# Kernel tuning notes

Hardware: AMD Instinct MI355X
Metric: run time of the kernel (lower is better)

The kernel has to match this reference:

```python
import jax, jax.numpy as jnp
import numpy as np
from jax import ops as jops

N = 20000          # nodes
E = 320000         # edges
IN_DIM = 16        # input_dim_features_extractor
HID = 64           # hidden_dim_features_extractor
HEADS = 4          # n_attention_heads
LAYERS = 2         # n_layers_features_extractor
NEG_SLOPE = 0.2    # DGL EGATConv leaky_relu slope


def setup_inputs() -> dict:
    key = jax.random.key(0)
    ks = jax.random.split(key, 16)
    s = lambda *sh: 1.0 / np.sqrt(sh[-2] if len(sh) >= 2 else sh[-1])
    inp = {
        "node_feat": jax.random.normal(ks[0], (N, IN_DIM), jnp.float32),
        "edge_feat": jax.random.normal(ks[1], (E, HID), jnp.float32),
        "src": jax.random.randint(ks[2], (E,), 0, N, jnp.int32),
        "dst": jax.random.randint(ks[3], (E,), 0, N, jnp.int32),
        # features_embedder (MLP n_layers=1 -> single Linear IN_DIM->HID)
        "W_embed": jax.random.normal(ks[4], (IN_DIM, HID), jnp.float32) * s(IN_DIM, HID),
        "b_embed": jnp.zeros((HID,), jnp.float32),
        # per-layer EGATConv params (stacked over layer dim)
        "W_ni": jax.random.normal(ks[5], (LAYERS, HID, HEADS * HID), jnp.float32) * s(HID, 1),
        "W_nj": jax.random.normal(ks[6], (LAYERS, HID, HEADS * HID), jnp.float32) * s(HID, 1),
        "W_fij": jax.random.normal(ks[7], (LAYERS, HID, HEADS * HID), jnp.float32) * s(HID, 1),
        "b_att": jnp.zeros((LAYERS, HEADS * HID), jnp.float32),
        "attn": jax.random.normal(ks[8], (LAYERS, HEADS, HID), jnp.float32) * s(HID),
        "W_node": jax.random.normal(ks[9], (LAYERS, HID, HEADS * HID), jnp.float32) * s(HID, 1),
        # per-layer MLP (n_layers=1 -> Linear HEADS*HID -> HID)
        "W_mlp": jax.random.normal(ks[10], (LAYERS, HEADS * HID, HID), jnp.float32) * s(HEADS * HID, 1),
        "b_mlp": jnp.zeros((LAYERS, HID), jnp.float32),
    }
    return inp


def _egat(h, f, src, dst, W_ni, W_nj, W_fij, b, attn, W_node):
    """DGL EGATConv: edge-feature attention + softmax-weighted aggregation."""
    # per-edge attention features: u_add_v + edge proj + bias
    f_ni = h @ W_ni                         # (N, H*D)
    f_nj = h @ W_nj                         # (N, H*D)
    f_fij = f @ W_fij                       # (E, H*D)
    f_out = f_ni[src] + f_nj[dst] + f_fij + b
    f_out = jax.nn.leaky_relu(f_out, NEG_SLOPE).reshape(E, HEADS, HID)
    e = jnp.einsum("ehd,hd->eh", f_out, attn)            # (E, H) logits
    # edge softmax over incoming edges of each dst node (numerically stable)
    m = jops.segment_max(e, dst, num_segments=N)          # (N, H)
    a = jnp.exp(e - m[dst])
    z = jops.segment_sum(a, dst, num_segments=N)          # (N, H)
    a = a / z[dst]
    # weighted message aggregation
    hn = (h @ W_node).reshape(N, HEADS, HID)
    msg = hn[src] * a[:, :, None]                         # (E, H, D)
    out = jops.segment_sum(msg, dst, num_segments=N)      # (N, H, D)
    return out


def reference(node_feat, edge_feat, src, dst, W_embed, b_embed,
              W_ni, W_nj, W_fij, b_att, attn, W_node, W_mlp, b_mlp):
    features_list = [node_feat]                 # layer_pooling='all'
    features = node_feat @ W_embed + b_embed    # features_embedder
    features_list.append(features)
    for L in range(LAYERS):
        h = _egat(features, edge_feat, src, dst,
                  W_ni[L], W_nj[L], W_fij[L], b_att[L], attn[L], W_node[L])
        new = h.reshape(N, HEADS * HID) @ W_mlp[L] + b_mlp[L]
        features = new + features               # residual
        features_list.append(features)
    return jnp.concatenate(features_list, axis=-1)   # (N, 16 + 3*64)
```

## Files before the change

kernel.cpp:

```cpp
#include <hip/hip_runtime.h>
#include <math.h>

#define NN 20000
#define NE 320000
#define IN_DIM 16
#define HID 64
#define HEADS 4
#define HD 256
#define OUTW 208
#define NEG 0.2f

typedef unsigned short u16;
typedef unsigned int u32;
typedef __attribute__((ext_vector_type(8))) short bf16x8;
typedef __attribute__((ext_vector_type(4))) float f32x4;

__device__ __forceinline__ float b2f(u16 u) {
  union { u32 i; float f; } c; c.i = ((u32)u) << 16; return c.f;
}
__device__ __forceinline__ u16 f2b(float f) {
  union { float f; u32 i; } c; c.f = f;
  u32 r = (c.i + 0x7FFFu + ((c.i >> 16) & 1u)) >> 16;
  return (u16)r;
}

__global__ void k_embed(const float* __restrict__ nf, const float* __restrict__ We,
                        const float* __restrict__ be, float* __restrict__ feat,
                        float* __restrict__ out) {
  int tid = blockIdx.x * blockDim.x + threadIdx.x;
  int n = tid >> 6, c = tid & 63;
  if (n >= NN) return;
  float acc = be[c];
#pragma unroll
  for (int k = 0; k < IN_DIM; ++k)
    acc += nf[n * IN_DIM + k] * We[k * HID + c];
  feat[n * HID + c] = acc;
  out[n * OUTW + 16 + c] = acc;
  if (c < IN_DIM) out[n * OUTW + c] = nf[n * IN_DIM + c];
}

__global__ void k_count(const int* __restrict__ dst, int* __restrict__ counts) {
  int e = blockIdx.x * blockDim.x + threadIdx.x;
  if (e < NE) atomicAdd(&counts[dst[e]], 1);
}

__global__ void k_scan(const int* __restrict__ counts, int* __restrict__ rowptr) {
  __shared__ int wsum[16];
  __shared__ int tot;
  int lane = threadIdx.x & 63, wid = threadIdx.x >> 6;
  int running = 0;
  if (threadIdx.x == 0) rowptr[0] = 0;
  for (int base = 0; base < NN; base += 1024) {
    int i = base + threadIdx.x;
    int x = (i < NN) ? counts[i] : 0;
#pragma unroll
    for (int d = 1; d < 64; d <<= 1) {
      int t = __shfl_up(x, d);
      if (lane >= d) x += t;
    }
    if (lane == 63) wsum[wid] = x;
    __syncthreads();
    if (wid == 0) {
      int wv = (lane < 16) ? wsum[lane] : 0;
#pragma unroll
      for (int d = 1; d < 16; d <<= 1) {
        int t = __shfl_up(wv, d);
        if (lane >= d) wv += t;
      }
      if (lane < 16) wsum[lane] = wv;
      if (lane == 15) tot = wv;
    }
    __syncthreads();
    int wpre = (wid == 0) ? 0 : wsum[wid - 1];
    if (i < NN) rowptr[i + 1] = running + wpre + x;
    running += tot;
    __syncthreads();
  }
}

__global__ void k_scatter(const int* __restrict__ dst, const int* __restrict__ src,
                          const int* __restrict__ rowptr, int* __restrict__ cursor,
                          int* __restrict__ eidx, int* __restrict__ srcp,
                          int* __restrict__ dstp) {
  int e = blockIdx.x * blockDim.x + threadIdx.x;
  if (e >= NE) return;
  int d = dst[e];
  int pos = rowptr[d] + atomicAdd(&cursor[d], 1);
  eidx[pos] = e;
  srcp[pos] = src[e];
  dstp[pos] = d;
}

__global__ void k_permute(const float* __restrict__ ef, const int* __restrict__ eidx,
                          u16* __restrict__ efbp) {
  int t = blockIdx.x * blockDim.x + threadIdx.x;
  int slot = t >> 4, c = (t & 15) * 4;
  int e = eidx[slot];
  float4 v = *reinterpret_cast<const float4*>(&ef[(size_t)e * HID + c]);
  ushort4 o;
  o.x = f2b(v.x); o.y = f2b(v.y); o.z = f2b(v.z); o.w = f2b(v.w);
  *reinterpret_cast<ushort4*>(&efbp[(size_t)slot * HID + c]) = o;
}

__global__ void k_prepw(const float* __restrict__ Wf, u16* __restrict__ Wt) {
  int tid = blockIdx.x * blockDim.x + threadIdx.x;
  int n = tid >> 6, k = tid & 63;
  if (n >= HD) return;
  Wt[n * HID + k] = f2b(Wf[k * HD + n]);
}

__global__ __launch_bounds__(256) void k_nodeproj(
    const float* __restrict__ feat, const float* __restrict__ Wni,
    const float* __restrict__ Wnj, const float* __restrict__ Wnd,
    const float* __restrict__ batt, u16* __restrict__ fni,
    u16* __restrict__ fnj, u16* __restrict__ hn) {
  __shared__ float hs[8 * HID];
  int n0 = blockIdx.x * 8;
  int c = threadIdx.x;
  for (int i = threadIdx.x; i < 8 * HID; i += 256)
    hs[i] = feat[(size_t)(n0 + (i >> 6)) * HID + (i & 63)];
  __syncthreads();
  float aI[8] = {0}, aJ[8] = {0}, aN[8] = {0};
  for (int k = 0; k < HID; ++k) {
    float wi = Wni[k * HD + c], wj = Wnj[k * HD + c], wn = Wnd[k * HD + c];
#pragma unroll
    for (int t = 0; t < 8; ++t) {
      float x = hs[t * HID + k];
      aI[t] += x * wi; aJ[t] += x * wj; aN[t] += x * wn;
    }
  }
  float b = batt[c];
#pragma unroll
  for (int t = 0; t < 8; ++t) {
    int n = n0 + t;
    fni[(size_t)n * HD + c] = f2b(aI[t] + b);
    fnj[(size_t)n * HD + c] = f2b(aJ[t]);
    hn[(size_t)n * HD + c]  = f2b(aN[t]);
  }
}

__global__ __launch_bounds__(256) void k_edgelogits(
    const u16* __restrict__ efbp, const int* __restrict__ srcp,
    const int* __restrict__ dstp, const u16* __restrict__ fni,
    const u16* __restrict__ fnj, const u16* __restrict__ Wt,
    const float* __restrict__ attnL, float* __restrict__ elog) {
  int h = threadIdx.x >> 6;
  int l = threadIdx.x & 63;
  int q = l >> 4;
  int n = l & 15;
  bf16x8 bfr[4][2];
#pragma unroll
  for (int nt = 0; nt < 4; ++nt)
#pragma unroll
    for (int kk = 0; kk < 2; ++kk)
      bfr[nt][kk] = *reinterpret_cast<const bf16x8*>(
          &Wt[(h * 64 + nt * 16 + n) * HID + kk * 32 + q * 8]);
  float at[4];
#pragma unroll
  for (int nt = 0; nt < 4; ++nt) at[nt] = attnL[h * 64 + nt * 16 + n];
  int tgt0 = n - 8 * q;
  int tgt1 = 16 + n - 8 * q;
  union { bf16x8 v; u32 w[4]; } uI0, uI1;
#pragma unroll
  for (int w4 = 0; w4 < 4; ++w4) {
    uI0.w[w4] = ((2 * w4 == tgt0) ? 0x3F80u : 0u) | ((2 * w4 + 1 == tgt0) ? 0x3F800000u : 0u);
    uI1.w[w4] = ((2 * w4 == tgt1) ? 0x3F80u : 0u) | ((2 * w4 + 1 == tgt1) ? 0x3F800000u : 0u);
  }
  bf16x8 bI0 = uI0.v, bI1 = uI1.v;

#define TILEMMA(aa0, aa1, fi0, fi1, fj0, fj1, ibase)                              \
  {                                                                               \
    float sumr[4] = {0.f, 0.f, 0.f, 0.f};                                         \
    _Pragma("unroll")                                                             \
    for (int nt = 0; nt < 4; ++nt) {                                              \
      f32x4 acc = {0.f, 0.f, 0.f, 0.f};                                           \
      acc = __builtin_amdgcn_mfma_f32_16x16x32_bf16(aa0, bfr[nt][0], acc, 0, 0, 0); \
      acc = __builtin_amdgcn_mfma_f32_16x16x32_bf16(aa1, bfr[nt][1], acc, 0, 0, 0); \
      acc = __builtin_amdgcn_mfma_f32_16x16x32_bf16((nt < 2) ? fi0 : fi1,         \
                                                    (nt & 1) ? bI1 : bI0, acc, 0, 0, 0); \
      acc = __builtin_amdgcn_mfma_f32_16x16x32_bf16((nt < 2) ? fj0 : fj1,         \
                                                    (nt & 1) ? bI1 : bI0, acc, 0, 0, 0); \
      _Pragma("unroll")                                                           \
      for (int r = 0; r < 4; ++r) {                                               \
        float v = acc[r];                                                         \
        v = v > 0.f ? v : NEG * v;                                                \
        sumr[r] += v * at[nt];                                                    \
      }                                                                           \
    }                                                                             \
    _Pragma("unroll")                                                             \
    for (int r = 0; r < 4; ++r) {                                                 \
      float v = sumr[r];                                                          \
      v += __shfl_xor(v, 1);                                                      \
      v += __shfl_xor(v, 2);                                                      \
      v += __shfl_xor(v, 4);                                                      \
      v += __shfl_xor(v, 8);                                                      \
      sumr[r] = v;                                                                \
    }                                                                             \
    if (n == 0) {                                                                 \
      float4 o_;                                                                  \
      o_.x = sumr[0]; o_.y = sumr[1]; o_.z = sumr[2]; o_.w = sumr[3];             \
      *reinterpret_cast<float4*>(&elog[(size_t)h * NE + (ibase) + q * 4]) = o_;   \
    }                                                                             \
  }

  const int NT = NE / 16;
  const int G = gridDim.x;
  for (int tile = blockIdx.x; tile < NT; tile += 2 * G) {
    int t1 = tile + G;
    int i0 = tile * 16;
    bf16x8 a00 = *reinterpret_cast<const bf16x8*>(&efbp[(size_t)(i0 + n) * HID + q * 8]);
    bf16x8 a01 = *reinterpret_cast<const bf16x8*>(&efbp[(size_t)(i0 + n) * HID + 32 + q * 8]);
    int sA = srcp[i0 + n], dA = dstp[i0 + n];
    bf16x8 fiA0 = *reinterpret_cast<const bf16x8*>(&fni[(size_t)sA * HD + h * 64 + q * 8]);
    bf16x8 fiA1 = *reinterpret_cast<const bf16x8*>(&fni[(size_t)sA * HD + h * 64 + 32 + q * 8]);
    bf16x8 fjA0 = *reinterpret_cast<const bf16x8*>(&fnj[(size_t)dA * HD + h * 64 + q * 8]);
    bf16x8 fjA1 = *reinterpret_cast<const bf16x8*>(&fnj[(size_t)dA * HD + h * 64 + 32 + q * 8]);
    int i1 = 0;
    bf16x8 a10 = {}, a11 = {};
    bf16x8 fiB0 = {}, fiB1 = {}, fjB0 = {}, fjB1 = {};
    bool has1 = (t1 < NT);
    if (has1) {
      i1 = t1 * 16;
      a10 = *reinterpret_cast<const bf16x8*>(&efbp[(size_t)(i1 + n) * HID + q * 8]);
      a11 = *reinterpret_cast<const bf16x8*>(&efbp[(size_t)(i1 + n) * HID + 32 + q * 8]);
      int sB = srcp[i1 + n], dB = dstp[i1 + n];
      fiB0 = *reinterpret_cast<const bf16x8*>(&fni[(size_t)sB * HD + h * 64 + q * 8]);
      fiB1 = *reinterpret_cast<const bf16x8*>(&fni[(size_t)sB * HD + h * 64 + 32 + q * 8]);
      fjB0 = *reinterpret_cast<const bf16x8*>(&fnj[(size_t)dB * HD + h * 64 + q * 8]);
      fjB1 = *reinterpret_cast<const bf16x8*>(&fnj[(size_t)dB * HD + h * 64 + 32 + q * 8]);
    }
    TILEMMA(a00, a01, fiA0, fiA1, fjA0, fjA1, i0);
    if (has1) {
      TILEMMA(a10, a11, fiB0, fiB1, fjB0, fjB1, i1);
    }
  }
#undef TILEMMA
}

__global__ __launch_bounds__(256) void k_agg(
    const int* __restrict__ rowptr, const int* __restrict__ srcp,
    const float* __restrict__ elog, const u16* __restrict__ hn,
    float* __restrict__ agg) {
  int n = (blockIdx.x * blockDim.x + threadIdx.x) >> 6;
  int j = threadIdx.x & 63;
  if (n >= NN) return;
  int s0 = rowptr[n], s1 = rowptr[n + 1];
  int h = j >> 4, u = j & 15;
  const float* er = elog + (size_t)h * NE;
  float m = -1e30f;
  for (int i = s0 + u; i < s1; i += 16) m = fmaxf(m, er[i]);
  m = fmaxf(m, __shfl_xor(m, 1));
  m = fmaxf(m, __shfl_xor(m, 2));
  m = fmaxf(m, __shfl_xor(m, 4));
  m = fmaxf(m, __shfl_xor(m, 8));
  float z = 0.f;
  for (int i = s0 + u; i < s1; i += 16) z += __expf(er[i] - m);
  z += __shfl_xor(z, 1);
  z += __shfl_xor(z, 2);
  z += __shfl_xor(z, 4);
  z += __shfl_xor(z, 8);
  float invz = (z > 0.f) ? 1.0f / z : 0.f;
  float4 ac[8];
#pragma unroll
  for (int t = 0; t < 8; ++t) ac[t] = make_float4(0, 0, 0, 0);
  int i = s0;
  for (; i + 8 <= s1; i += 8) {
    int sv[8]; float wv[8]; ushort4 vv[8];
#pragma unroll
    for (int t = 0; t < 8; ++t) sv[t] = srcp[i + t];
#pragma unroll
    for (int t = 0; t < 8; ++t) wv[t] = __expf(er[i + t] - m) * invz;
#pragma unroll
    for (int t = 0; t < 8; ++t)
      vv[t] = *reinterpret_cast<const ushort4*>(&hn[(size_t)sv[t] * HD + 4 * j]);
#pragma unroll
    for (int t = 0; t < 8; ++t) {
      ac[t].x += b2f(vv[t].x) * wv[t]; ac[t].y += b2f(vv[t].y) * wv[t];
      ac[t].z += b2f(vv[t].z) * wv[t]; ac[t].w += b2f(vv[t].w) * wv[t];
    }
  }
  for (; i < s1; ++i) {
    int s = srcp[i];
    float w = __expf(er[i] - m) * invz;
    ushort4 v = *reinterpret_cast<const ushort4*>(&hn[(size_t)s * HD + 4 * j]);
    ac[0].x += b2f(v.x) * w; ac[0].y += b2f(v.y) * w;
    ac[0].z += b2f(v.z) * w; ac[0].w += b2f(v.w) * w;
  }
  float4 acc;
  acc.x = ((ac[0].x + ac[1].x) + (ac[2].x + ac[3].x)) + ((ac[4].x + ac[5].x) + (ac[6].x + ac[7].x));
  acc.y = ((ac[0].y + ac[1].y) + (ac[2].y + ac[3].y)) + ((ac[4].y + ac[5].y) + (ac[6].y + ac[7].y));
  acc.z = ((ac[0].z + ac[1].z) + (ac[2].z + ac[3].z)) + ((ac[4].z + ac[5].z) + (ac[6].z + ac[7].z));
  acc.w = ((ac[0].w + ac[1].w) + (ac[2].w + ac[3].w)) + ((ac[4].w + ac[5].w) + (ac[6].w + ac[7].w));
  *reinterpret_cast<float4*>(&agg[(size_t)n * HD + 4 * j]) = acc;
}

__global__ __launch_bounds__(256) void k_mlp(
    const float* __restrict__ agg, const float* __restrict__ Wm,
    const float* __restrict__ bm, float* __restrict__ feat,
    float* __restrict__ out, int outoff) {
  __shared__ float as_[32 * HD];
  int n0 = blockIdx.x * 32;
  for (int i = threadIdx.x; i < 32 * HD; i += 256) as_[i] = agg[(size_t)n0 * HD + i];
  __syncthreads();
  int c = threadIdx.x & 63;
  int g = threadIdx.x >> 6;
  float acc[8] = {0};
  for (int k = 0; k < HD; ++k) {
    float wv = Wm[k * HID + c];
#pragma unroll
    for (int t = 0; t < 8; ++t)
      acc[t] += as_[(g * 8 + t) * HD + k] * wv;
  }
  float b = bm[c];
#pragma unroll
  for (int t = 0; t < 8; ++t) {
    int n = n0 + g * 8 + t;
    float v = acc[t] + b + feat[n * HID + c];
    feat[n * HID + c] = v;
    out[n * OUTW + outoff + c] = v;
  }
}

extern "C" void kernel_launch(void* const* d_in, const int* in_sizes, int n_in,
                              void* d_out, int out_size, void* d_ws, size_t ws_size,
                              hipStream_t stream) {
  const float* node_feat = (const float*)d_in[0];
  const float* edge_feat = (const float*)d_in[1];
  const int*   src       = (const int*)d_in[2];
  const int*   dst       = (const int*)d_in[3];
  const float* W_embed   = (const float*)d_in[4];
  const float* b_embed   = (const float*)d_in[5];
  const float* W_ni      = (const float*)d_in[6];
  const float* W_nj      = (const float*)d_in[7];
  const float* W_fij     = (const float*)d_in[8];
  const float* b_att     = (const float*)d_in[9];
  const float* attn      = (const float*)d_in[10];
  const float* W_node    = (const float*)d_in[11];
  const float* W_mlp     = (const float*)d_in[12];
  const float* b_mlp     = (const float*)d_in[13];
  float* out = (float*)d_out;

  float* ws   = (float*)d_ws;
  float* feat = ws;
  u16*  fni   = (u16*)(feat + (size_t)NN * HID);
  u16*  fnj   = fni + (size_t)NN * HD;
  u16*  hn    = fnj + (size_t)NN * HD;
  u16*  efbp  = hn + (size_t)NN * HD;
  u16*  Wt    = efbp + (size_t)NE * HID;
  float* elog = (float*)(Wt + (size_t)HD * HID);
  int* counts = (int*)(elog + (size_t)NE * HEADS);
  int* rowptr = counts + NN;
  int* cursor = rowptr + NN + 1;
  int* eidx   = cursor + NN;
  int* srcp   = eidx + NE;
  int* dstp   = srcp + NE;
  float* aggb = (float*)fni;

  hipMemsetAsync(counts, 0, sizeof(int) * NN, stream);
  hipMemsetAsync(cursor, 0, sizeof(int) * NN, stream);

  k_embed<<<(NN * 64) / 256, 256, 0, stream>>>(node_feat, W_embed, b_embed, feat, out);
  k_count<<<NE / 256, 256, 0, stream>>>(dst, counts);
  k_scan<<<1, 1024, 0, stream>>>(counts, rowptr);
  k_scatter<<<NE / 256, 256, 0, stream>>>(dst, src, rowptr, cursor, eidx, srcp, dstp);
  k_permute<<<(NE * 16) / 256, 256, 0, stream>>>(edge_feat, eidx, efbp);

  for (int L = 0; L < 2; ++L) {
    const float* WniL = W_ni + (size_t)L * HID * HD;
    const float* WnjL = W_nj + (size_t)L * HID * HD;
    const float* WfL  = W_fij + (size_t)L * HID * HD;
    const float* WndL = W_node + (size_t)L * HID * HD;
    const float* battL = b_att + (size_t)L * HD;
    const float* attnL = attn + (size_t)L * HEADS * HID;
    const float* WmL  = W_mlp + (size_t)L * HD * HID;
    const float* bmL  = b_mlp + (size_t)L * HID;

    k_prepw<<<(HID * HD) / 256, 256, 0, stream>>>(WfL, Wt);
    k_nodeproj<<<NN / 8, 256, 0, stream>>>(feat, WniL, WnjL, WndL, battL, fni, fnj, hn);
    k_edgelogits<<<2048, 256, 0, stream>>>(efbp, srcp, dstp, fni, fnj, Wt, attnL, elog);
    k_agg<<<(NN * 64) / 256, 256, 0, stream>>>(rowptr, srcp, elog, hn, aggb);
    k_mlp<<<NN / 32, 256, 0, stream>>>(aggb, WmL, bmL, feat, out, 80 + L * 64);
  }
}
```

Before: 555.5 us.

## Fuse setup kernels, triple-buffer edge logits, widen aggregation gathers

Merges embed with degree counting, and edge-feature permutation with both layers' weight transposes, into single launches. The cursor memset is dropped; the scan kernel zeroes the cursor array instead. The edge-logit kernel now prefetches three tiles per iteration on half the grid to expose more memory-level parallelism. The aggregation kernel splits each warp into two halves that process alternating edges with 16-byte bf16 loads, then combines them with a cross-half shuffle, cutting load instruction count at the cost of extra shuffles and register use.

Measured after the change: 572.2 us. 3.0% more time.

```diff
diff --git a/kernel.cpp b/kernel.cpp
--- a/kernel.cpp
+++ b/kernel.cpp
@@ -13,6 +13,7 @@
 typedef unsigned short u16;
 typedef unsigned int u32;
 typedef __attribute__((ext_vector_type(8))) short bf16x8;
+typedef __attribute__((ext_vector_type(8))) unsigned short u16x8;
 typedef __attribute__((ext_vector_type(4))) float f32x4;
 
 __device__ __forceinline__ float b2f(u16 u) {
@@ -24,27 +25,30 @@
   return (u16)r;
 }
 
-__global__ void k_embed(const float* __restrict__ nf, const float* __restrict__ We,
-                        const float* __restrict__ be, float* __restrict__ feat,
-                        float* __restrict__ out) {
-  int tid = blockIdx.x * blockDim.x + threadIdx.x;
-  int n = tid >> 6, c = tid & 63;
-  if (n >= NN) return;
-  float acc = be[c];
-#pragma unroll
-  for (int k = 0; k < IN_DIM; ++k)
-    acc += nf[n * IN_DIM + k] * We[k * HID + c];
-  feat[n * HID + c] = acc;
-  out[n * OUTW + 16 + c] = acc;
-  if (c < IN_DIM) out[n * OUTW + c] = nf[n * IN_DIM + c];
-}
-
-__global__ void k_count(const int* __restrict__ dst, int* __restrict__ counts) {
-  int e = blockIdx.x * blockDim.x + threadIdx.x;
-  if (e < NE) atomicAdd(&counts[dst[e]], 1);
-}
-
-__global__ void k_scan(const int* __restrict__ counts, int* __restrict__ rowptr) {
+__global__ void k_embed_count(const float* __restrict__ nf, const float* __restrict__ We,
+                              const float* __restrict__ be, float* __restrict__ feat,
+                              float* __restrict__ out, const int* __restrict__ dst,
+                              int* __restrict__ counts) {
+  int bid = blockIdx.x;
+  const int EB = (NN * 64) / 256;
+  if (bid < EB) {
+    int tid = bid * 256 + threadIdx.x;
+    int n = tid >> 6, c = tid & 63;
+    float acc = be[c];
+#pragma unroll
+    for (int k = 0; k < IN_DIM; ++k)
+      acc += nf[n * IN_DIM + k] * We[k * HID + c];
+    feat[n * HID + c] = acc;
+    out[n * OUTW + 16 + c] = acc;
+    if (c < IN_DIM) out[n * OUTW + c] = nf[n * IN_DIM + c];
+  } else {
+    int e = (bid - EB) * 256 + threadIdx.x;
+    if (e < NE) atomicAdd(&counts[dst[e]], 1);
+  }
+}
+
+__global__ void k_scan(const int* __restrict__ counts, int* __restrict__ rowptr,
+                       int* __restrict__ cursor) {
   __shared__ int wsum[16];
   __shared__ int tot;
   int lane = threadIdx.x & 63, wid = threadIdx.x >> 6;
@@ -53,6 +57,7 @@
   for (int base = 0; base < NN; base += 1024) {
     int i = base + threadIdx.x;
     int x = (i < NN) ? counts[i] : 0;
+    if (i < NN) cursor[i] = 0;
 #pragma unroll
     for (int d = 1; d < 64; d <<= 1) {
       int t = __shfl_up(x, d);
@@ -91,22 +96,27 @@
   dstp[pos] = d;
 }
 
-__global__ void k_permute(const float* __restrict__ ef, const int* __restrict__ eidx,
-                          u16* __restrict__ efbp) {
-  int t = blockIdx.x * blockDim.x + threadIdx.x;
-  int slot = t >> 4, c = (t & 15) * 4;
-  int e = eidx[slot];
-  float4 v = *reinterpret_cast<const float4*>(&ef[(size_t)e * HID + c]);
-  ushort4 o;
-  o.x = f2b(v.x); o.y = f2b(v.y); o.z = f2b(v.z); o.w = f2b(v.w);
-  *reinterpret_cast<ushort4*>(&efbp[(size_t)slot * HID + c]) = o;
-}
-
-__global__ void k_prepw(const float* __restrict__ Wf, u16* __restrict__ Wt) {
-  int tid = blockIdx.x * blockDim.x + threadIdx.x;
-  int n = tid >> 6, k = tid & 63;
-  if (n >= HD) return;
-  Wt[n * HID + k] = f2b(Wf[k * HD + n]);
+__global__ void k_permute_prepw(const float* __restrict__ ef, const int* __restrict__ eidx,
+                                u16* __restrict__ efbp, const float* __restrict__ Wf,
+                                u16* __restrict__ Wt0, u16* __restrict__ Wt1) {
+  int bid = blockIdx.x;
+  const int PB = (NE * 16) / 256;
+  if (bid < PB) {
+    int t = bid * 256 + threadIdx.x;
+    int slot = t >> 4, c = (t & 15) * 4;
+    int e = eidx[slot];
+    float4 v = *reinterpret_cast<const float4*>(&ef[(size_t)e * HID + c]);
+    ushort4 o;
+    o.x = f2b(v.x); o.y = f2b(v.y); o.z = f2b(v.z); o.w = f2b(v.w);
+    *reinterpret_cast<ushort4*>(&efbp[(size_t)slot * HID + c]) = o;
+  } else {
+    int r = (bid - PB) * 256 + threadIdx.x;
+    int Lw = r >> 14;
+    int idx = r & 16383;
+    int nn2 = idx >> 6, kk2 = idx & 63;
+    u16* WtL = Lw ? Wt1 : Wt0;
+    WtL[nn2 * HID + kk2] = f2b(Wf[(size_t)Lw * HID * HD + kk2 * HD + nn2]);
+  }
 }
 
 __global__ __launch_bounds__(256) void k_nodeproj(
@@ -205,34 +215,26 @@
 
   const int NT = NE / 16;
   const int G = gridDim.x;
-  for (int tile = blockIdx.x; tile < NT; tile += 2 * G) {
-    int t1 = tile + G;
-    int i0 = tile * 16;
-    bf16x8 a00 = *reinterpret_cast<const bf16x8*>(&efbp[(size_t)(i0 + n) * HID + q * 8]);
-    bf16x8 a01 = *reinterpret_cast<const bf16x8*>(&efbp[(size_t)(i0 + n) * HID + 32 + q * 8]);
-    int sA = srcp[i0 + n], dA = dstp[i0 + n];
-    bf16x8 fiA0 = *reinterpret_cast<const bf16x8*>(&fni[(size_t)sA * HD + h * 64 + q * 8]);
-    bf16x8 fiA1 = *reinterpret_cast<const bf16x8*>(&fni[(size_t)sA * HD + h * 64 + 32 + q * 8]);
-    bf16x8 fjA0 = *reinterpret_cast<const bf16x8*>(&fnj[(size_t)dA * HD + h * 64 + q * 8]);
-    bf16x8 fjA1 = *reinterpret_cast<const bf16x8*>(&fnj[(size_t)dA * HD + h * 64 + 32 + q * 8]);
-    int i1 = 0;
-    bf16x8 a10 = {}, a11 = {};
-    bf16x8 fiB0 = {}, fiB1 = {}, fjB0 = {}, fjB1 = {};
-    bool has1 = (t1 < NT);
-    if (has1) {
-      i1 = t1 * 16;
-      a10 = *reinterpret_cast<const bf16x8*>(&efbp[(size_t)(i1 + n) * HID + q * 8]);
-      a11 = *reinterpret_cast<const bf16x8*>(&efbp[(size_t)(i1 + n) * HID + 32 + q * 8]);
-      int sB = srcp[i1 + n], dB = dstp[i1 + n];
-      fiB0 = *reinterpret_cast<const bf16x8*>(&fni[(size_t)sB * HD + h * 64 + q * 8]);
-      fiB1 = *reinterpret_cast<const bf16x8*>(&fni[(size_t)sB * HD + h * 64 + 32 + q * 8]);
-      fjB0 = *reinterpret_cast<const bf16x8*>(&fnj[(size_t)dB * HD + h * 64 + q * 8]);
-      fjB1 = *reinterpret_cast<const bf16x8*>(&fnj[(size_t)dB * HD + h * 64 + 32 + q * 8]);
-    }
-    TILEMMA(a00, a01, fiA0, fiA1, fjA0, fjA1, i0);
-    if (has1) {
-      TILEMMA(a10, a11, fiB0, fiB1, fjB0, fjB1, i1);
-    }
+  for (int t0 = blockIdx.x; t0 < NT; t0 += 3 * G) {
+    bf16x8 A0[3], A1[3], FI0[3], FI1[3], FJ0[3], FJ1[3];
+    int ib[3];
+#pragma unroll
+    for (int k = 0; k < 3; ++k) {
+      int t = t0 + k * G;
+      int tc = (t < NT) ? t : (NT - 1);
+      ib[k] = (t < NT) ? tc * 16 : -1;
+      int i0 = tc * 16;
+      A0[k] = *reinterpret_cast<const bf16x8*>(&efbp[(size_t)(i0 + n) * HID + q * 8]);
+      A1[k] = *reinterpret_cast<const bf16x8*>(&efbp[(size_t)(i0 + n) * HID + 32 + q * 8]);
+      int s = srcp[i0 + n], d = dstp[i0 + n];
+      FI0[k] = *reinterpret_cast<const bf16x8*>(&fni[(size_t)s * HD + h * 64 + q * 8]);
+      FI1[k] = *reinterpret_cast<const bf16x8*>(&fni[(size_t)s * HD + h * 64 + 32 + q * 8]);
+      FJ0[k] = *reinterpret_cast<const bf16x8*>(&fnj[(size_t)d * HD + h * 64 + q * 8]);
+      FJ1[k] = *reinterpret_cast<const bf16x8*>(&fnj[(size_t)d * HD + h * 64 + 32 + q * 8]);
+    }
+#pragma unroll
+    for (int k = 0; k < 3; ++k)
+      if (ib[k] >= 0) TILEMMA(A0[k], A1[k], FI0[k], FI1[k], FJ0[k], FJ1[k], ib[k]);
   }
 #undef TILEMMA
 }
@@ -245,53 +247,59 @@
   int j = threadIdx.x & 63;
   if (n >= NN) return;
   int s0 = rowptr[n], s1 = rowptr[n + 1];
-  int h = j >> 4, u = j & 15;
-  const float* er = elog + (size_t)h * NE;
+  int half = j >> 5;
+  int lo = j & 31;
+  int hA = (j >> 3) & 3;
+  int u = (j & 7) + 8 * half;
+  const float* er = elog + (size_t)hA * NE;
   float m = -1e30f;
   for (int i = s0 + u; i < s1; i += 16) m = fmaxf(m, er[i]);
   m = fmaxf(m, __shfl_xor(m, 1));
   m = fmaxf(m, __shfl_xor(m, 2));
   m = fmaxf(m, __shfl_xor(m, 4));
-  m = fmaxf(m, __shfl_xor(m, 8));
+  m = fmaxf(m, __shfl_xor(m, 32));
   float z = 0.f;
   for (int i = s0 + u; i < s1; i += 16) z += __expf(er[i] - m);
   z += __shfl_xor(z, 1);
   z += __shfl_xor(z, 2);
   z += __shfl_xor(z, 4);
-  z += __shfl_xor(z, 8);
+  z += __shfl_xor(z, 32);
   float invz = (z > 0.f) ? 1.0f / z : 0.f;
-  float4 ac[8];
-#pragma unroll
-  for (int t = 0; t < 8; ++t) ac[t] = make_float4(0, 0, 0, 0);
+  float a8[8] = {0.f, 0.f, 0.f, 0.f, 0.f, 0.f, 0.f, 0.f};
   int i = s0;
   for (; i + 8 <= s1; i += 8) {
-    int sv[8]; float wv[8]; ushort4 vv[8];
+    int sv[8]; float wv[8];
 #pragma unroll
     for (int t = 0; t < 8; ++t) sv[t] = srcp[i + t];
 #pragma unroll
     for (int t = 0; t < 8; ++t) wv[t] = __expf(er[i + t] - m) * invz;
-#pragma unroll
-    for (int t = 0; t < 8; ++t)
-      vv[t] = *reinterpret_cast<const ushort4*>(&hn[(size_t)sv[t] * HD + 4 * j]);
-#pragma unroll
-    for (int t = 0; t < 8; ++t) {
-      ac[t].x += b2f(vv[t].x) * wv[t]; ac[t].y += b2f(vv[t].y) * wv[t];
-      ac[t].z += b2f(vv[t].z) * wv[t]; ac[t].w += b2f(vv[t].w) * wv[t];
+    u16x8 vv[4];
+#pragma unroll
+    for (int g = 0; g < 4; ++g)
+      vv[g] = *reinterpret_cast<const u16x8*>(&hn[(size_t)sv[2 * g + half] * HD + 8 * lo]);
+#pragma unroll
+    for (int g = 0; g < 4; ++g) {
+      float w = wv[2 * g + half];
+#pragma unroll
+      for (int e = 0; e < 8; ++e) a8[e] += b2f(vv[g][e]) * w;
     }
   }
   for (; i < s1; ++i) {
     int s = srcp[i];
-    float w = __expf(er[i] - m) * invz;
-    ushort4 v = *reinterpret_cast<const ushort4*>(&hn[(size_t)s * HD + 4 * j]);
-    ac[0].x += b2f(v.x) * w; ac[0].y += b2f(v.y) * w;
-    ac[0].z += b2f(v.z) * w; ac[0].w += b2f(v.w) * w;
-  }
-  float4 acc;
-  acc.x = ((ac[0].x + ac[1].x) + (ac[2].x + ac[3].x)) + ((ac[4].x + ac[5].x) + (ac[6].x + ac[7].x));
-  acc.y = ((ac[0].y + ac[1].y) + (ac[2].y + ac[3].y)) + ((ac[4].y + ac[5].y) + (ac[6].y + ac[7].y));
-  acc.z = ((ac[0].z + ac[1].z) + (ac[2].z + ac[3].z)) + ((ac[4].z + ac[5].z) + (ac[6].z + ac[7].z));
-  acc.w = ((ac[0].w + ac[1].w) + (ac[2].w + ac[3].w)) + ((ac[4].w + ac[5].w) + (ac[6].w + ac[7].w));
-  *reinterpret_cast<float4*>(&agg[(size_t)n * HD + 4 * j]) = acc;
+    float w = half ? 0.f : (__expf(er[i] - m) * invz);
+    u16x8 v = *reinterpret_cast<const u16x8*>(&hn[(size_t)s * HD + 8 * lo]);
+#pragma unroll
+    for (int e = 0; e < 8; ++e) a8[e] += b2f(v[e]) * w;
+  }
+#pragma unroll
+  for (int e = 0; e < 8; ++e) a8[e] += __shfl_xor(a8[e], 32);
+  if (j < 32) {
+    float4 o0, o1;
+    o0.x = a8[0]; o0.y = a8[1]; o0.z = a8[2]; o0.w = a8[3];
+    o1.x = a8[4]; o1.y = a8[5]; o1.z = a8[6]; o1.w = a8[7];
+    *reinterpret_cast<float4*>(&agg[(size_t)n * HD + 8 * lo]) = o0;
+    *reinterpret_cast<float4*>(&agg[(size_t)n * HD + 8 * lo + 4]) = o1;
+  }
 }
 
 __global__ __launch_bounds__(256) void k_mlp(
@@ -346,8 +354,9 @@
   u16*  fnj   = fni + (size_t)NN * HD;
   u16*  hn    = fnj + (size_t)NN * HD;
   u16*  efbp  = hn + (size_t)NN * HD;
-  u16*  Wt    = efbp + (size_t)NE * HID;
-  float* elog = (float*)(Wt + (size_t)HD * HID);
+  u16*  Wt0   = efbp + (size_t)NE * HID;
+  u16*  Wt1   = Wt0 + (size_t)HD * HID;
+  float* elog = (float*)(Wt1 + (size_t)HD * HID);
   int* counts = (int*)(elog + (size_t)NE * HEADS);
   int* rowptr = counts + NN;
   int* cursor = rowptr + NN + 1;
@@ -357,27 +366,26 @@
   float* aggb = (float*)fni;
 
   hipMemsetAsync(counts, 0, sizeof(int) * NN, stream);
-  hipMemsetAsync(cursor, 0, sizeof(int) * NN, stream);
-
-  k_embed<<<(NN * 64) / 256, 256, 0, stream>>>(node_feat, W_embed, b_embed, feat, out);
-  k_count<<<NE / 256, 256, 0, stream>>>(dst, counts);
-  k_scan<<<1, 1024, 0, stream>>>(counts, rowptr);
+
+  k_embed_count<<<(NN * 64) / 256 + NE / 256, 256, 0, stream>>>(
+      node_feat, W_embed, b_embed, feat, out, dst, counts);
+  k_scan<<<1, 1024, 0, stream>>>(counts, rowptr, cursor);
   k_scatter<<<NE / 256, 256, 0, stream>>>(dst, src, rowptr, cursor, eidx, srcp, dstp);
-  k_permute<<<(NE * 16) / 256, 256, 0, stream>>>(edge_feat, eidx, efbp);
+  k_permute_prepw<<<(NE * 16) / 256 + 128, 256, 0, stream>>>(
+      edge_feat, eidx, efbp, W_fij, Wt0, Wt1);
 
   for (int L = 0; L < 2; ++L) {
     const float* WniL = W_ni + (size_t)L * HID * HD;
     const float* WnjL = W_nj + (size_t)L * HID * HD;
-    const float* WfL  = W_fij + (size_t)L * HID * HD;
     const float* WndL = W_node + (size_t)L * HID * HD;
     const float* battL = b_att + (size_t)L * HD;
     const float* attnL = attn + (size_t)L * HEADS * HID;
     const float* WmL  = W_mlp + (size_t)L * HD * HID;
     const float* bmL  = b_mlp + (size_t)L * HID;
-
-    k_prepw<<<(HID * HD) / 256, 256, 0, stream>>>(WfL, Wt);
+    u16* WtL = L ? Wt1 : Wt0;
+
     k_nodeproj<<<NN / 8, 256, 0, stream>>>(feat, WniL, WnjL, WndL, battL, fni, fnj, hn);
-    k_edgelogits<<<2048, 256, 0, stream>>>(efbp, srcp, dstp, fni, fnj, Wt, attnL, elog);
+    k_edgelogits<<<1024, 256, 0, stream>>>(efbp, srcp, dstp, fni, fnj, WtL, attnL, elog);
     k_agg<<<(NN * 64) / 256, 256, 0, stream>>>(rowptr, srcp, elog, hn, aggb);
     k_mlp<<<NN / 32, 256, 0, stream>>>(aggb, WmL, bmL, feat, out, 80 + L * 64);
   }
```
